# Kernel optimization log

Measured on AMD Instinct MI355X. Metric: run time of the kernel, lower is better.

Reference implementation:

```python
import jax, jax.numpy as jnp
import numpy as np

# OGB feature vocab sizes
ATOM_DIMS = [119, 4, 12, 12, 10, 6, 6, 2, 2]
BOND_DIMS = [5, 6, 2]
ATOM_OFF = np.concatenate([[0], np.cumsum(ATOM_DIMS)[:-1]]).astype(np.int32)
BOND_OFF = np.concatenate([[0], np.cumsum(BOND_DIMS)[:-1]]).astype(np.int32)
SCHEDULE_LEN = 5   # len(train_schedule) == len(eval_schedule)
NUM_GRAPHS = 12000
BN_EPS = 1e-5

N_NODES, N_EDGES, HIDDEN, NUM_TASKS = 300000, 600000, 128, 128


def setup_inputs() -> dict:
    key = jax.random.key(0)
    ks = jax.random.split(key, 16)
    x = jax.random.randint(ks[0], (N_NODES, 9), 0, 2, dtype=jnp.int32)
    edge_index = jax.random.randint(ks[1], (2, N_EDGES), 0, N_NODES, dtype=jnp.int32)
    edge_attr = jax.random.randint(ks[2], (N_EDGES, 3), 0, 2, dtype=jnp.int32)
    batch = jnp.sort(jax.random.randint(ks[3], (N_NODES,), 0, NUM_GRAPHS, dtype=jnp.int32))
    # learned parameters (embedding tables concatenated with offsets)
    atom_emb = jax.random.normal(ks[4], (sum(ATOM_DIMS), HIDDEN), jnp.float32) * 0.1
    bond_emb = jax.random.normal(ks[5], (sum(BOND_DIMS), HIDDEN), jnp.float32) * 0.1
    conv_W = jax.random.normal(ks[6], (HIDDEN, HIDDEN), jnp.float32) * (1.0 / np.sqrt(HIDDEN))
    conv_b = jnp.zeros((HIDDEN,), jnp.float32)
    root_emb = jax.random.normal(ks[7], (HIDDEN,), jnp.float32) * 0.1
    bn_gamma = jnp.ones((HIDDEN,), jnp.float32)
    bn_beta = jnp.zeros((HIDDEN,), jnp.float32)
    bn_mean = jnp.zeros((HIDDEN,), jnp.float32)   # running stats (eval mode)
    bn_var = jnp.ones((HIDDEN,), jnp.float32)
    lin_W = jax.random.normal(ks[8], (NUM_TASKS, HIDDEN), jnp.float32) * (1.0 / np.sqrt(HIDDEN))
    lin_b = jnp.zeros((NUM_TASKS,), jnp.float32)
    return {"x": x, "edge_index": edge_index, "edge_attr": edge_attr, "batch": batch,
            "atom_emb": atom_emb, "bond_emb": bond_emb, "conv_W": conv_W, "conv_b": conv_b,
            "root_emb": root_emb, "bn_gamma": bn_gamma, "bn_beta": bn_beta,
            "bn_mean": bn_mean, "bn_var": bn_var, "lin_W": lin_W, "lin_b": lin_b}


def reference(x, edge_index, edge_attr, batch, atom_emb, bond_emb, conv_W, conv_b,
              root_emb, bn_gamma, bn_beta, bn_mean, bn_var, lin_W, lin_b):
    N = x.shape[0]
    # AtomEncoder / BondEncoder: sum of per-feature embedding lookups
    h = atom_emb[x + jnp.asarray(ATOM_OFF, x.dtype)].sum(axis=1)            # [N, H]
    e = bond_emb[edge_attr + jnp.asarray(BOND_OFF, edge_attr.dtype)].sum(axis=1)  # [E, H]
    row, col = edge_index[0], edge_index[1]
    deg = jax.ops.segment_sum(jnp.ones_like(row, h.dtype), row, num_segments=N) + 1.0  # [N]
    dis = deg ** -0.5                                                        # deg >= 1, no inf
    norm = dis[row] * dis[col]                                               # [E]
    inv_std = bn_gamma / jnp.sqrt(bn_var + BN_EPS)
    for i in range(SCHEDULE_LEN):
        old = h
        z = h @ conv_W.T + conv_b                                            # [N, H]
        # message: norm * relu(x_j + edge_emb), aggregated at target (col) via scatter-add
        msg = norm[:, None] * jax.nn.relu(z[row] + e)                        # [E, H]
        agg = jax.ops.segment_sum(msg, col, num_segments=N)                  # [N, H]
        z = agg + jax.nn.relu(z + root_emb) / deg[:, None]                   # self-loop term
        z = jax.nn.relu(z)
        z = (z - bn_mean) * inv_std + bn_beta                                # BN (eval, running stats)
        # dropout: identity in eval mode
        # NOTE: faithful to source bug: smooth_fac is the loop index i, not schedule[i]
        h = i * old + (1 - i) * z
    # global mean pool over graphs
    counts = jax.ops.segment_sum(jnp.ones((N,), h.dtype), batch, num_segments=NUM_GRAPHS)
    pooled = jax.ops.segment_sum(h, batch, num_segments=NUM_GRAPHS) / jnp.maximum(counts, 1.0)[:, None]
    return pooled @ lin_W.T + lin_b                                          # [num_graphs, num_tasks]
```

## Files before the change

kernel.cpp:

```cpp
#include <hip/hip_runtime.h>

#define HID 128

typedef __attribute__((ext_vector_type(8))) short short8;
typedef __attribute__((ext_vector_type(8))) unsigned short ushort8v;
typedef __attribute__((ext_vector_type(4))) float floatx4;
typedef __attribute__((ext_vector_type(4))) unsigned short ushort4v;

__device__ __forceinline__ unsigned short f2bf(float f) {
    unsigned u = __builtin_bit_cast(unsigned, f);
    u += 0x7FFF + ((u >> 16) & 1);
    return (unsigned short)(u >> 16);
}
__device__ __forceinline__ float bf2f(unsigned short s) {
    unsigned u = ((unsigned)s) << 16;
    return __builtin_bit_cast(float, u);
}

__global__ void diag_kernel(float* __restrict__ out, long n, float val)
{
    long i = (long)blockIdx.x * blockDim.x + threadIdx.x;
    if (i < n) out[i] = val;
}

__global__ __launch_bounds__(256) void prep_kernel(
    float* __restrict__ dis, int* __restrict__ indeg, int N,
    const float* __restrict__ conv_W, unsigned short* __restrict__ Wb,
    const float* __restrict__ lin_W, unsigned short* __restrict__ linWb,
    const float* __restrict__ bond_emb, float* __restrict__ comb,
    const float* __restrict__ gamma, const float* __restrict__ beta,
    const float* __restrict__ mean, const float* __restrict__ var,
    float* __restrict__ bnsc, float* __restrict__ bnsh,
    const int* __restrict__ batch, int* __restrict__ gptr, int G, int B)
{
    int blk = blockIdx.x;
    int tid = threadIdx.x;
    if (blk < B) {
        int i = blk * 256 + tid;
        if (i < N) { dis[i] = 0.f; indeg[i] = 0; }
    } else if (blk < B + 64) {
        int i = (blk - B) * 256 + tid;
        Wb[i] = f2bf(conv_W[i]);
    } else if (blk < B + 128) {
        int i = (blk - B - 64) * 256 + tid;
        linWb[i] = f2bf(lin_W[i]);
    } else if (blk < B + 158) {
        int i = (blk - B - 128) * 2 + (tid >> 7);
        int c = tid & 127;
        int a0 = i / 12, a1 = (i % 12) / 2, a2 = i % 2;
        comb[i * HID + c] = bond_emb[a0 * HID + c] + bond_emb[(5 + a1) * HID + c]
                          + bond_emb[(11 + a2) * HID + c];
    } else if (blk == B + 158) {
        if (tid < HID) {
            float sc = gamma[tid] * rsqrtf(var[tid] + 1e-5f);
            bnsc[tid] = sc;
            bnsh[tid] = beta[tid] - mean[tid] * sc;
        }
    } else {
        int n = (blk - B - 159) * 256 + tid;
        if (n < N) {
            int b = batch[n];
            int bp = (n == 0) ? -1 : batch[n - 1];
            for (int g = bp + 1; g <= b; ++g) gptr[g] = n;
            if (n == N - 1)
                for (int g = b + 1; g <= G; ++g) gptr[g] = N;
        }
    }
}

__global__ void hist_kernel(const int* __restrict__ ei, float* __restrict__ dis,
                            int* __restrict__ indeg, int E)
{
    for (int e = blockIdx.x * blockDim.x + threadIdx.x; e < E; e += gridDim.x * blockDim.x) {
        atomicAdd(&dis[ei[e]], 1.f);
        atomicAdd(&indeg[ei[E + e]], 1);
    }
}

__global__ __launch_bounds__(256) void postdeg_kernel(
    float* __restrict__ dis, const int* __restrict__ indeg,
    int* __restrict__ partial, int N)
{
    __shared__ int s[256];
    int i = blockIdx.x * 256 + threadIdx.x;
    if (i < N) dis[i] = rsqrtf(dis[i] + 1.f);
    s[threadIdx.x] = (i < N) ? indeg[i] : 0;
    __syncthreads();
    for (int d = 128; d > 0; d >>= 1) {
        if (threadIdx.x < d) s[threadIdx.x] += s[threadIdx.x + d];
        __syncthreads();
    }
    if (threadIdx.x == 0) partial[blockIdx.x] = s[0];
}

__global__ __launch_bounds__(256) void scan1_kernel(
    const int* __restrict__ partial, int* __restrict__ offs,
    int* __restrict__ ptr, int B, int N)
{
    __shared__ int s[256];
    __shared__ int carry_s;
    int tid = threadIdx.x;
    if (tid == 0) carry_s = 0;
    __syncthreads();
    for (int base = 0; base < B; base += 256) {
        int i = base + tid;
        int v = (i < B) ? partial[i] : 0;
        s[tid] = v;
        __syncthreads();
        for (int d = 1; d < 256; d <<= 1) {
            int t = (tid >= d) ? s[tid - d] : 0;
            __syncthreads();
            s[tid] += t;
            __syncthreads();
        }
        int carry = carry_s;
        if (i < B) offs[i] = carry + s[tid] - v;
        __syncthreads();
        if (tid == 0) carry_s = carry + s[255];
        __syncthreads();
    }
    if (tid == 0) ptr[N] = carry_s;
}

__global__ __launch_bounds__(256) void scan2_kernel(
    const int* __restrict__ indeg, const int* __restrict__ offs,
    int* __restrict__ ptr, int* __restrict__ cursor, int N)
{
    __shared__ int s[256];
    int tid = threadIdx.x;
    int i = blockIdx.x * 256 + tid;
    int v = (i < N) ? indeg[i] : 0;
    s[tid] = v;
    __syncthreads();
    for (int d = 1; d < 256; d <<= 1) {
        int t = (tid >= d) ? s[tid - d] : 0;
        __syncthreads();
        s[tid] += t;
        __syncthreads();
    }
    if (i < N) {
        int ex = offs[blockIdx.x] + s[tid] - v;
        ptr[i] = ex;
        cursor[i] = ex;
    }
}

__global__ void fillcsr_kernel(const int* __restrict__ ei, const int* __restrict__ attr,
                               const float* __restrict__ dis, int* __restrict__ cursor,
                               int2* __restrict__ edata, int E)
{
    for (int e = blockIdx.x * blockDim.x + threadIdx.x; e < E; e += gridDim.x * blockDim.x) {
        int r   = ei[e];
        int col = ei[E + e];
        int pos = atomicAdd(&cursor[col], 1);
        int ci  = attr[e * 3] * 12 + attr[e * 3 + 1] * 2 + attr[e * 3 + 2];
        float nrm = dis[r] * dis[col];
        int2 ed;
        ed.x = r;
        ed.y = ci | ((int)f2bf(nrm) << 16);
        edata[pos] = ed;
    }
}

template<bool FIRST>
__device__ __forceinline__ ushort8v agg_node(
    long n, int c, const int* __restrict__ ptr, const int2* __restrict__ edata,
    const float* __restrict__ comb, const float* __restrict__ dis,
    const float* __restrict__ root, const float* __restrict__ bnsc,
    const float* __restrict__ bnsh, const unsigned short* __restrict__ zb,
    const unsigned short* __restrict__ hb, float fi)
{
    ushort8v zv = *reinterpret_cast<const ushort8v*>(zb + n * HID + c);
    ushort8v hv;
    if constexpr (!FIRST) hv = *reinterpret_cast<const ushort8v*>(hb + n * HID + c);
    float di = dis[n];
    float rd = di * di;
    float acc[8];
#pragma unroll
    for (int j = 0; j < 8; ++j) acc[j] = fmaxf(bf2f(zv[j]) + root[c + j], 0.f) * rd;

    int jb = ptr[n], je = ptr[n + 1];
    int j2 = jb;
    for (; j2 + 1 < je; j2 += 2) {
        int2 e0 = edata[j2];
        int2 e1 = edata[j2 + 1];
        ushort8v z0 = *reinterpret_cast<const ushort8v*>(zb + (long)e0.x * HID + c);
        ushort8v z1 = *reinterpret_cast<const ushort8v*>(zb + (long)e1.x * HID + c);
        const float* c0 = comb + (e0.y & 0xFF) * HID + c;
        const float* c1 = comb + (e1.y & 0xFF) * HID + c;
        float n0 = bf2f((unsigned short)(((unsigned)e0.y) >> 16));
        float n1 = bf2f((unsigned short)(((unsigned)e1.y) >> 16));
#pragma unroll
        for (int j = 0; j < 8; ++j) {
            acc[j] += fmaxf(bf2f(z0[j]) + c0[j], 0.f) * n0;
            acc[j] += fmaxf(bf2f(z1[j]) + c1[j], 0.f) * n1;
        }
    }
    if (j2 < je) {
        int2 e0 = edata[j2];
        ushort8v z0 = *reinterpret_cast<const ushort8v*>(zb + (long)e0.x * HID + c);
        const float* c0 = comb + (e0.y & 0xFF) * HID + c;
        float n0 = bf2f((unsigned short)(((unsigned)e0.y) >> 16));
#pragma unroll
        for (int j = 0; j < 8; ++j) acc[j] += fmaxf(bf2f(z0[j]) + c0[j], 0.f) * n0;
    }

    ushort8v o;
#pragma unroll
    for (int j = 0; j < 8; ++j) {
        float t = fmaxf(acc[j], 0.f) * bnsc[c + j] + bnsh[c + j];
        float h;
        if constexpr (FIRST) h = t;
        else h = fi * bf2f(hv[j]) + (1.f - fi) * t;
        o[j] = f2bf(h);
    }
    return o;
}

template<bool FIRST>
__global__ __launch_bounds__(256) void agg_kernel(
    const int* __restrict__ ptr, const int2* __restrict__ edata,
    const float* __restrict__ comb, const float* __restrict__ dis,
    const float* __restrict__ root, const float* __restrict__ bnsc,
    const float* __restrict__ bnsh, const unsigned short* __restrict__ zb,
    unsigned short* __restrict__ hb, float fi, int N)
{
    long n = (long)blockIdx.x * 16 + (threadIdx.x >> 4);
    if (n >= N) return;
    int c = (threadIdx.x & 15) * 8;
    ushort8v o = agg_node<FIRST>(n, c, ptr, edata, comb, dis, root, bnsc, bnsh, zb, hb, fi);
    *reinterpret_cast<ushort8v*>(hb + n * HID + c) = o;
}

__global__ __launch_bounds__(256) void gemm_kernel(
    const unsigned short* __restrict__ hb, const unsigned short* __restrict__ Wb,
    const float* __restrict__ bias, unsigned short* __restrict__ zb, int N)
{
    __shared__ unsigned short st[4][32][144];
    int tid = threadIdx.x;
    int wave = tid >> 6;
    int lane = tid & 63;
    int l15 = lane & 15;
    int q = lane >> 4;
    long row0 = (long)blockIdx.x * 128 + wave * 32;

    short8 a[2][4];
#pragma unroll
    for (int mt = 0; mt < 2; ++mt) {
        long rl = row0 + mt * 16 + l15;
        if (rl > (long)N - 1) rl = (long)N - 1;
        const unsigned short* ap = hb + rl * HID + q * 8;
#pragma unroll
        for (int kb = 0; kb < 4; ++kb)
            a[mt][kb] = *reinterpret_cast<const short8*>(ap + kb * 32);
    }

    floatx4 acc[2][8];
#pragma unroll
    for (int mt = 0; mt < 2; ++mt)
#pragma unroll
        for (int nt = 0; nt < 8; ++nt) {
            floatx4 zz = {0.f, 0.f, 0.f, 0.f};
            acc[mt][nt] = zz;
        }

#pragma unroll
    for (int nt = 0; nt < 8; ++nt) {
        const unsigned short* bp = Wb + (nt * 16 + l15) * HID + q * 8;
#pragma unroll
        for (int kb = 0; kb < 4; ++kb) {
            short8 b = *reinterpret_cast<const short8*>(bp + kb * 32);
            acc[0][nt] = __builtin_amdgcn_mfma_f32_16x16x32_bf16(a[0][kb], b, acc[0][nt], 0, 0, 0);
            acc[1][nt] = __builtin_amdgcn_mfma_f32_16x16x32_bf16(a[1][kb], b, acc[1][nt], 0, 0, 0);
        }
    }

    float bi[8];
#pragma unroll
    for (int nt = 0; nt < 8; ++nt) bi[nt] = bias[nt * 16 + l15];

#pragma unroll
    for (int mt = 0; mt < 2; ++mt)
#pragma unroll
        for (int r = 0; r < 4; ++r) {
            int lr = mt * 16 + q * 4 + r;
#pragma unroll
            for (int nt = 0; nt < 8; ++nt)
                st[wave][lr][l15 + 16 * nt] = f2bf(acc[mt][nt][r] + bi[nt]);
        }

#pragma unroll
    for (int it = 0; it < 8; ++it) {
        int lr = it * 4 + q;
        long gr = row0 + lr;
        if (gr < N) {
            ushort8v v = *reinterpret_cast<const ushort8v*>(&st[wave][lr][l15 * 8]);
            *reinterpret_cast<ushort8v*>(zb + gr * HID + l15 * 8) = v;
        }
    }
}

__global__ __launch_bounds__(256) void egemm_kernel(
    const int* __restrict__ x, const float* __restrict__ atom_emb,
    const unsigned short* __restrict__ Wb, const float* __restrict__ bias,
    unsigned short* __restrict__ zb, int N)
{
    __shared__ unsigned short st[4][32][144];
    int tid = threadIdx.x;
    int wave = tid >> 6;
    int lane = tid & 63;
    int l15 = lane & 15;
    int q = lane >> 4;
    long row0 = (long)blockIdx.x * 128 + wave * 32;
    const int OFF[9] = {0, 119, 123, 135, 147, 157, 163, 169, 171};

    int cc = l15 * 8;
#pragma unroll 1
    for (int s = 0; s < 8; ++s) {
        int lr = s * 4 + q;
        long n = row0 + lr;
        ushort8v o;
        if (n < N) {
            float acc[8];
#pragma unroll
            for (int j = 0; j < 8; ++j) acc[j] = 0.f;
#pragma unroll
            for (int f = 0; f < 9; ++f) {
                int idx = x[n * 9 + f] + OFF[f];
                const float* ep = atom_emb + (long)idx * HID + cc;
                floatx4 v0 = *reinterpret_cast<const floatx4*>(ep);
                floatx4 v1 = *reinterpret_cast<const floatx4*>(ep + 4);
#pragma unroll
                for (int j = 0; j < 4; ++j) { acc[j] += v0[j]; acc[j + 4] += v1[j]; }
            }
#pragma unroll
            for (int j = 0; j < 8; ++j) o[j] = f2bf(acc[j]);
        } else {
            ushort8v z8 = {0, 0, 0, 0, 0, 0, 0, 0};
            o = z8;
        }
        *reinterpret_cast<ushort8v*>(&st[wave][lr][cc]) = o;
    }

    short8 a[2][4];
#pragma unroll
    for (int mt = 0; mt < 2; ++mt) {
        int rl = mt * 16 + l15;
#pragma unroll
        for (int kb = 0; kb < 4; ++kb)
            a[mt][kb] = *reinterpret_cast<const short8*>(&st[wave][rl][q * 8 + kb * 32]);
    }

    floatx4 acc[2][8];
#pragma unroll
    for (int mt = 0; mt < 2; ++mt)
#pragma unroll
        for (int nt = 0; nt < 8; ++nt) {
            floatx4 zz = {0.f, 0.f, 0.f, 0.f};
            acc[mt][nt] = zz;
        }

#pragma unroll
    for (int nt = 0; nt < 8; ++nt) {
        const unsigned short* bp = Wb + (nt * 16 + l15) * HID + q * 8;
#pragma unroll
        for (int kb = 0; kb < 4; ++kb) {
            short8 b = *reinterpret_cast<const short8*>(bp + kb * 32);
            acc[0][nt] = __builtin_amdgcn_mfma_f32_16x16x32_bf16(a[0][kb], b, acc[0][nt], 0, 0, 0);
            acc[1][nt] = __builtin_amdgcn_mfma_f32_16x16x32_bf16(a[1][kb], b, acc[1][nt], 0, 0, 0);
        }
    }

    float bi[8];
#pragma unroll
    for (int nt = 0; nt < 8; ++nt) bi[nt] = bias[nt * 16 + l15];

#pragma unroll
    for (int mt = 0; mt < 2; ++mt)
#pragma unroll
        for (int r = 0; r < 4; ++r) {
            int lr = mt * 16 + q * 4 + r;
#pragma unroll
            for (int nt = 0; nt < 8; ++nt)
                st[wave][lr][l15 + 16 * nt] = f2bf(acc[mt][nt][r] + bi[nt]);
        }

#pragma unroll
    for (int it = 0; it < 8; ++it) {
        int lr = it * 4 + q;
        long gr = row0 + lr;
        if (gr < N) {
            ushort8v v = *reinterpret_cast<const ushort8v*>(&st[wave][lr][l15 * 8]);
            *reinterpret_cast<ushort8v*>(zb + gr * HID + l15 * 8) = v;
        }
    }
}

__global__ __launch_bounds__(256) void linmm_kernel(
    const unsigned short* __restrict__ pb, const unsigned short* __restrict__ Wb,
    const float* __restrict__ bias, float* __restrict__ out, int G)
{
    int wave = threadIdx.x >> 6;
    int lane = threadIdx.x & 63;
    int l15 = lane & 15;
    int q = lane >> 4;
    long row0 = (long)blockIdx.x * 128 + wave * 32;

    short8 a[2][4];
#pragma unroll
    for (int mt = 0; mt < 2; ++mt) {
        long rl = row0 + mt * 16 + l15;
        if (rl > (long)G - 1) rl = (long)G - 1;
        const unsigned short* ap = pb + rl * HID + q * 8;
#pragma unroll
        for (int kb = 0; kb < 4; ++kb)
            a[mt][kb] = *reinterpret_cast<const short8*>(ap + kb * 32);
    }

    floatx4 acc[2][8];
#pragma unroll
    for (int mt = 0; mt < 2; ++mt)
#pragma unroll
        for (int nt = 0; nt < 8; ++nt) {
            floatx4 zz = {0.f, 0.f, 0.f, 0.f};
            acc[mt][nt] = zz;
        }

#pragma unroll
    for (int nt = 0; nt < 8; ++nt) {
        const unsigned short* bp = Wb + (nt * 16 + l15) * HID + q * 8;
#pragma unroll
        for (int kb = 0; kb < 4; ++kb) {
            short8 b = *reinterpret_cast<const short8*>(bp + kb * 32);
            acc[0][nt] = __builtin_amdgcn_mfma_f32_16x16x32_bf16(a[0][kb], b, acc[0][nt], 0, 0, 0);
            acc[1][nt] = __builtin_amdgcn_mfma_f32_16x16x32_bf16(a[1][kb], b, acc[1][nt], 0, 0, 0);
        }
    }

    float bi[8];
#pragma unroll
    for (int nt = 0; nt < 8; ++nt) bi[nt] = bias[nt * 16 + l15];

#pragma unroll
    for (int mt = 0; mt < 2; ++mt)
#pragma unroll
        for (int r = 0; r < 4; ++r) {
            long rr = row0 + mt * 16 + q * 4 + r;
            if (rr < G) {
                float* op = out + rr * HID + l15;
#pragma unroll
                for (int nt = 0; nt < 8; ++nt)
                    op[nt * 16] = acc[mt][nt][r] + bi[nt];
            }
        }
}

__global__ __launch_bounds__(256) void pool_kernel(
    const unsigned short* __restrict__ hb, const int* __restrict__ gptr,
    unsigned short* __restrict__ pb, int G)
{
    int g = blockIdx.x;
    if (g >= G) return;
    int tid = threadIdx.x;
    int sub = tid >> 5;
    int c = (tid & 31) * 4;
    int lo = gptr[g], hi = gptr[g + 1];
    floatx4 s = {0.f, 0.f, 0.f, 0.f};
    for (int n = lo + sub; n < hi; n += 8) {
        ushort4v hv = *reinterpret_cast<const ushort4v*>(hb + (long)n * HID + c);
#pragma unroll
        for (int j = 0; j < 4; ++j) s[j] += bf2f(hv[j]);
    }
    __shared__ float ps[8][HID];
    *reinterpret_cast<floatx4*>(&ps[sub][c]) = s;
    __syncthreads();
    if (tid < HID) {
        float sum = 0.f;
#pragma unroll
        for (int k = 0; k < 8; ++k) sum += ps[k][tid];
        float cnt = (hi > lo) ? (float)(hi - lo) : 1.f;
        pb[(long)g * HID + tid] = f2bf(sum / cnt);
    }
}

extern "C" void kernel_launch(void* const* d_in, const int* in_sizes, int n_in,
                              void* d_out, int out_size, void* d_ws, size_t ws_size,
                              hipStream_t stream)
{
    const int* x          = (const int*)d_in[0];
    const int* ei         = (const int*)d_in[1];
    const int* attr       = (const int*)d_in[2];
    const int* batch      = (const int*)d_in[3];
    const float* atom_emb = (const float*)d_in[4];
    const float* bond_emb = (const float*)d_in[5];
    const float* conv_W   = (const float*)d_in[6];
    const float* conv_b   = (const float*)d_in[7];
    const float* root     = (const float*)d_in[8];
    const float* gamma    = (const float*)d_in[9];
    const float* beta     = (const float*)d_in[10];
    const float* mean     = (const float*)d_in[11];
    const float* var      = (const float*)d_in[12];
    const float* lin_W    = (const float*)d_in[13];
    const float* lin_b    = (const float*)d_in[14];
    float* out = (float*)d_out;

    const int N = in_sizes[0] / 9;
    const int E = in_sizes[1] / 2;
    const int G = out_size / HID;
    const int B = (N + 255) / 256;

    auto al = [](size_t b) { return (b + 255) & ~(size_t)255; };
    const size_t need =
        al((size_t)N * HID * 2) +
        al((size_t)N * HID * 2) +
        al((size_t)(N + 1) * 4) +
        al((size_t)E * 8) +
        al((size_t)N * 4) +
        al((size_t)2048 * 4) * 2 +
        al((size_t)(G + 1) * 4) +
        al((size_t)(G + 128) * HID * 2) +
        al((size_t)60 * HID * 4) +
        al((size_t)HID * 4) * 2 +
        al((size_t)HID * HID * 2) * 2;

    if (ws_size < need || B > 2048) {
        float v = (B > 2048) ? 3000.f : (1000.f + (float)(ws_size >> 20));
        long n = (long)out_size;
        diag_kernel<<<(int)((n + 255) / 256), 256, 0, stream>>>(out, n, v);
        return;
    }

    char* wsp = (char*)d_ws;
    size_t used = 0;
    auto alloc = [&](size_t bytes) { char* p = wsp + used; used += al(bytes); return p; };
    unsigned short* hb = (unsigned short*)alloc((size_t)N * HID * 2);
    unsigned short* zb = (unsigned short*)alloc((size_t)N * HID * 2);
    int* ptr      = (int*)alloc((size_t)(N + 1) * 4);
    int2* edata   = (int2*)alloc((size_t)E * 8);
    int* indeg    = (int*)alloc((size_t)N * 4);
    int* cursor   = indeg;
    int* partial  = (int*)alloc((size_t)2048 * 4);
    int* offs     = (int*)alloc((size_t)2048 * 4);
    int* gptr     = (int*)alloc((size_t)(G + 1) * 4);
    unsigned short* pb = (unsigned short*)alloc((size_t)(G + 128) * HID * 2);
    float* dis    = (float*)pb;
    float* comb   = (float*)alloc((size_t)60 * HID * 4);
    float* bnsc   = (float*)alloc((size_t)HID * 4);
    float* bnsh   = (float*)alloc((size_t)HID * 4);
    unsigned short* Wb    = (unsigned short*)alloc((size_t)HID * HID * 2);
    unsigned short* linWb = (unsigned short*)alloc((size_t)HID * HID * 2);

    prep_kernel<<<2 * B + 159, 256, 0, stream>>>(dis, indeg, N, conv_W, Wb, lin_W, linWb,
                                                 bond_emb, comb, gamma, beta, mean, var,
                                                 bnsc, bnsh, batch, gptr, G, B);
    hist_kernel<<<1024, 256, 0, stream>>>(ei, dis, indeg, E);
    postdeg_kernel<<<B, 256, 0, stream>>>(dis, indeg, partial, N);
    scan1_kernel<<<1, 256, 0, stream>>>(partial, offs, ptr, B, N);
    scan2_kernel<<<B, 256, 0, stream>>>(indeg, offs, ptr, cursor, N);
    fillcsr_kernel<<<1024, 256, 0, stream>>>(ei, attr, dis, cursor, edata, E);

    const int gemm_blocks = (N + 127) / 128;
    const int agg_blocks  = (N + 15) / 16;
    egemm_kernel<<<gemm_blocks, 256, 0, stream>>>(x, atom_emb, Wb, conv_b, zb, N);
    agg_kernel<true ><<<agg_blocks, 256, 0, stream>>>(ptr, edata, comb, dis, root,
            bnsc, bnsh, zb, hb, 0.f, N);
    const float fis[3] = {2.f, 3.f, 4.f};
    for (int t = 0; t < 3; ++t) {
        gemm_kernel<<<gemm_blocks, 256, 0, stream>>>(hb, Wb, conv_b, zb, N);
        agg_kernel<false><<<agg_blocks, 256, 0, stream>>>(ptr, edata, comb, dis, root,
                bnsc, bnsh, zb, hb, fis[t], N);
    }

    pool_kernel<<<G, 256, 0, stream>>>(hb, gptr, pb, G);
    linmm_kernel<<<(G + 127) / 128, 256, 0, stream>>>(pb, linWb, lin_b, out, G);
}
```

Before: 728.7 us.

## Permute hidden channel layout so MFMA results store directly without LDS transpose

```diff
diff --git a/kernel.cpp b/kernel.cpp
--- a/kernel.cpp
+++ b/kernel.cpp
@@ -1,6 +1,7 @@
 #include <hip/hip_runtime.h>
 
 #define HID 128
+#define ATOT 173
 
 typedef __attribute__((ext_vector_type(8))) short short8;
 typedef __attribute__((ext_vector_type(8))) unsigned short ushort8v;
@@ -16,6 +17,7 @@
     unsigned u = ((unsigned)s) << 16;
     return __builtin_bit_cast(float, u);
 }
+__device__ __forceinline__ int chact(int c) { return (c & 7) * 16 + (c >> 3); }
 
 __global__ void diag_kernel(float* __restrict__ out, long n, float val)
 {
@@ -31,6 +33,8 @@
     const float* __restrict__ gamma, const float* __restrict__ beta,
     const float* __restrict__ mean, const float* __restrict__ var,
     float* __restrict__ bnsc, float* __restrict__ bnsh,
+    const float* __restrict__ root, float* __restrict__ rootp,
+    const float* __restrict__ atom_emb, float* __restrict__ embp,
     const int* __restrict__ batch, int* __restrict__ gptr, int G, int B)
 {
     int blk = blockIdx.x;
@@ -40,24 +44,35 @@
         if (i < N) { dis[i] = 0.f; indeg[i] = 0; }
     } else if (blk < B + 64) {
         int i = (blk - B) * 256 + tid;
-        Wb[i] = f2bf(conv_W[i]);
+        int f = i >> 7, k = i & 127;
+        Wb[i] = f2bf(conv_W[f * HID + chact(k)]);
     } else if (blk < B + 128) {
         int i = (blk - B - 64) * 256 + tid;
-        linWb[i] = f2bf(lin_W[i]);
+        int t = i >> 7, k = i & 127;
+        linWb[i] = f2bf(lin_W[t * HID + chact(k)]);
     } else if (blk < B + 158) {
         int i = (blk - B - 128) * 2 + (tid >> 7);
         int c = tid & 127;
+        int ac = chact(c);
         int a0 = i / 12, a1 = (i % 12) / 2, a2 = i % 2;
-        comb[i * HID + c] = bond_emb[a0 * HID + c] + bond_emb[(5 + a1) * HID + c]
-                          + bond_emb[(11 + a2) * HID + c];
+        comb[i * HID + c] = bond_emb[a0 * HID + ac] + bond_emb[(5 + a1) * HID + ac]
+                          + bond_emb[(11 + a2) * HID + ac];
     } else if (blk == B + 158) {
         if (tid < HID) {
-            float sc = gamma[tid] * rsqrtf(var[tid] + 1e-5f);
+            int ac = chact(tid);
+            float sc = gamma[ac] * rsqrtf(var[ac] + 1e-5f);
             bnsc[tid] = sc;
-            bnsh[tid] = beta[tid] - mean[tid] * sc;
+            bnsh[tid] = beta[ac] - mean[ac] * sc;
+            rootp[tid] = root[ac];
+        }
+    } else if (blk < B + 246) {
+        int i = (blk - B - 159) * 256 + tid;
+        if (i < ATOT * HID) {
+            int r = i >> 7, c = i & 127;
+            embp[i] = atom_emb[r * HID + chact(c)];
         }
     } else {
-        int n = (blk - B - 159) * 256 + tid;
+        int n = (blk - B - 246) * 256 + tid;
         if (n < N) {
             int b = batch[n];
             int bp = (n == 0) ? -1 : batch[n - 1];
@@ -166,7 +181,7 @@
 __device__ __forceinline__ ushort8v agg_node(
     long n, int c, const int* __restrict__ ptr, const int2* __restrict__ edata,
     const float* __restrict__ comb, const float* __restrict__ dis,
-    const float* __restrict__ root, const float* __restrict__ bnsc,
+    const float* __restrict__ rootp, const float* __restrict__ bnsc,
     const float* __restrict__ bnsh, const unsigned short* __restrict__ zb,
     const unsigned short* __restrict__ hb, float fi)
 {
@@ -177,7 +192,7 @@
     float rd = di * di;
     float acc[8];
 #pragma unroll
-    for (int j = 0; j < 8; ++j) acc[j] = fmaxf(bf2f(zv[j]) + root[c + j], 0.f) * rd;
+    for (int j = 0; j < 8; ++j) acc[j] = fmaxf(bf2f(zv[j]) + rootp[c + j], 0.f) * rd;
 
     int jb = ptr[n], je = ptr[n + 1];
     int j2 = jb;
@@ -221,14 +236,14 @@
 __global__ __launch_bounds__(256) void agg_kernel(
     const int* __restrict__ ptr, const int2* __restrict__ edata,
     const float* __restrict__ comb, const float* __restrict__ dis,
-    const float* __restrict__ root, const float* __restrict__ bnsc,
+    const float* __restrict__ rootp, const float* __restrict__ bnsc,
     const float* __restrict__ bnsh, const unsigned short* __restrict__ zb,
     unsigned short* __restrict__ hb, float fi, int N)
 {
     long n = (long)blockIdx.x * 16 + (threadIdx.x >> 4);
     if (n >= N) return;
     int c = (threadIdx.x & 15) * 8;
-    ushort8v o = agg_node<FIRST>(n, c, ptr, edata, comb, dis, root, bnsc, bnsh, zb, hb, fi);
+    ushort8v o = agg_node<FIRST>(n, c, ptr, edata, comb, dis, rootp, bnsc, bnsh, zb, hb, fi);
     *reinterpret_cast<ushort8v*>(hb + n * HID + c) = o;
 }
 
@@ -236,7 +251,6 @@
     const unsigned short* __restrict__ hb, const unsigned short* __restrict__ Wb,
     const float* __restrict__ bias, unsigned short* __restrict__ zb, int N)
 {
-    __shared__ unsigned short st[4][32][144];
     int tid = threadIdx.x;
     int wave = tid >> 6;
     int lane = tid & 63;
@@ -283,29 +297,21 @@
     for (int mt = 0; mt < 2; ++mt)
 #pragma unroll
         for (int r = 0; r < 4; ++r) {
-            int lr = mt * 16 + q * 4 + r;
-#pragma unroll
-            for (int nt = 0; nt < 8; ++nt)
-                st[wave][lr][l15 + 16 * nt] = f2bf(acc[mt][nt][r] + bi[nt]);
-        }
-
-#pragma unroll
-    for (int it = 0; it < 8; ++it) {
-        int lr = it * 4 + q;
-        long gr = row0 + lr;
-        if (gr < N) {
-            ushort8v v = *reinterpret_cast<const ushort8v*>(&st[wave][lr][l15 * 8]);
-            *reinterpret_cast<ushort8v*>(zb + gr * HID + l15 * 8) = v;
-        }
-    }
+            long gr = row0 + mt * 16 + q * 4 + r;
+            if (gr < N) {
+                ushort8v o;
+#pragma unroll
+                for (int nt = 0; nt < 8; ++nt) o[nt] = f2bf(acc[mt][nt][r] + bi[nt]);
+                *reinterpret_cast<ushort8v*>(zb + gr * HID + l15 * 8) = o;
+            }
+        }
 }
 
 __global__ __launch_bounds__(256) void egemm_kernel(
-    const int* __restrict__ x, const float* __restrict__ atom_emb,
+    const int* __restrict__ x, const float* __restrict__ embp,
     const unsigned short* __restrict__ Wb, const float* __restrict__ bias,
     unsigned short* __restrict__ zb, int N)
 {
-    __shared__ unsigned short st[4][32][144];
     int tid = threadIdx.x;
     int wave = tid >> 6;
     int lane = tid & 63;
@@ -314,41 +320,38 @@
     long row0 = (long)blockIdx.x * 128 + wave * 32;
     const int OFF[9] = {0, 119, 123, 135, 147, 157, 163, 169, 171};
 
-    int cc = l15 * 8;
-#pragma unroll 1
-    for (int s = 0; s < 8; ++s) {
-        int lr = s * 4 + q;
-        long n = row0 + lr;
-        ushort8v o;
-        if (n < N) {
-            float acc[8];
-#pragma unroll
-            for (int j = 0; j < 8; ++j) acc[j] = 0.f;
-#pragma unroll
-            for (int f = 0; f < 9; ++f) {
-                int idx = x[n * 9 + f] + OFF[f];
-                const float* ep = atom_emb + (long)idx * HID + cc;
-                floatx4 v0 = *reinterpret_cast<const floatx4*>(ep);
-                floatx4 v1 = *reinterpret_cast<const floatx4*>(ep + 4);
-#pragma unroll
-                for (int j = 0; j < 4; ++j) { acc[j] += v0[j]; acc[j + 4] += v1[j]; }
+    short8 a[2][4];
+#pragma unroll
+    for (int mt = 0; mt < 2; ++mt) {
+        long rl = row0 + mt * 16 + l15;
+        if (rl > (long)N - 1) rl = (long)N - 1;
+        int xr[9];
+#pragma unroll
+        for (int f = 0; f < 9; ++f) xr[f] = x[rl * 9 + f] + OFF[f];
+        float s[32];
+#pragma unroll
+        for (int j = 0; j < 32; ++j) s[j] = 0.f;
+#pragma unroll
+        for (int f = 0; f < 9; ++f) {
+            const float* ep = embp + (long)xr[f] * HID + q * 8;
+#pragma unroll
+            for (int kb = 0; kb < 4; ++kb) {
+                floatx4 v0 = *reinterpret_cast<const floatx4*>(ep + kb * 32);
+                floatx4 v1 = *reinterpret_cast<const floatx4*>(ep + kb * 32 + 4);
+#pragma unroll
+                for (int j = 0; j < 4; ++j) {
+                    s[kb * 8 + j]     += v0[j];
+                    s[kb * 8 + 4 + j] += v1[j];
+                }
             }
-#pragma unroll
-            for (int j = 0; j < 8; ++j) o[j] = f2bf(acc[j]);
-        } else {
-            ushort8v z8 = {0, 0, 0, 0, 0, 0, 0, 0};
-            o = z8;
-        }
-        *reinterpret_cast<ushort8v*>(&st[wave][lr][cc]) = o;
-    }
-
-    short8 a[2][4];
-#pragma unroll
-    for (int mt = 0; mt < 2; ++mt) {
-        int rl = mt * 16 + l15;
-#pragma unroll
-        for (int kb = 0; kb < 4; ++kb)
-            a[mt][kb] = *reinterpret_cast<const short8*>(&st[wave][rl][q * 8 + kb * 32]);
+        }
+#pragma unroll
+        for (int kb = 0; kb < 4; ++kb) {
+            short8 v;
+#pragma unroll
+            for (int j = 0; j < 8; ++j) v[j] = (short)f2bf(s[kb * 8 + j]);
+            a[mt][kb] = v;
+        }
     }
 
     floatx4 acc[2][8];
@@ -379,21 +382,14 @@
     for (int mt = 0; mt < 2; ++mt)
 #pragma unroll
         for (int r = 0; r < 4; ++r) {
-            int lr = mt * 16 + q * 4 + r;
-#pragma unroll
-            for (int nt = 0; nt < 8; ++nt)
-                st[wave][lr][l15 + 16 * nt] = f2bf(acc[mt][nt][r] + bi[nt]);
-        }
-
-#pragma unroll
-    for (int it = 0; it < 8; ++it) {
-        int lr = it * 4 + q;
-        long gr = row0 + lr;
-        if (gr < N) {
-            ushort8v v = *reinterpret_cast<const ushort8v*>(&st[wave][lr][l15 * 8]);
-            *reinterpret_cast<ushort8v*>(zb + gr * HID + l15 * 8) = v;
-        }
-    }
+            long gr = row0 + mt * 16 + q * 4 + r;
+            if (gr < N) {
+                ushort8v o;
+#pragma unroll
+                for (int nt = 0; nt < 8; ++nt) o[nt] = f2bf(acc[mt][nt][r] + bi[nt]);
+                *reinterpret_cast<ushort8v*>(zb + gr * HID + l15 * 8) = o;
+            }
+        }
 }
 
 __global__ __launch_bounds__(256) void linmm_kernel(
@@ -520,7 +516,8 @@
         al((size_t)(G + 1) * 4) +
         al((size_t)(G + 128) * HID * 2) +
         al((size_t)60 * HID * 4) +
-        al((size_t)HID * 4) * 2 +
+        al((size_t)HID * 4) * 3 +
+        al((size_t)ATOT * HID * 4) +
         al((size_t)HID * HID * 2) * 2;
 
     if (ws_size < need || B > 2048) {
@@ -547,12 +544,15 @@
     float* comb   = (float*)alloc((size_t)60 * HID * 4);
     float* bnsc   = (float*)alloc((size_t)HID * 4);
     float* bnsh   = (float*)alloc((size_t)HID * 4);
+    float* rootp  = (float*)alloc((size_t)HID * 4);
+    float* embp   = (float*)alloc((size_t)ATOT * HID * 4);
     unsigned short* Wb    = (unsigned short*)alloc((size_t)HID * HID * 2);
     unsigned short* linWb = (unsigned short*)alloc((size_t)HID * HID * 2);
 
-    prep_kernel<<<2 * B + 159, 256, 0, stream>>>(dis, indeg, N, conv_W, Wb, lin_W, linWb,
+    prep_kernel<<<2 * B + 246, 256, 0, stream>>>(dis, indeg, N, conv_W, Wb, lin_W, linWb,
                                                  bond_emb, comb, gamma, beta, mean, var,
-                                                 bnsc, bnsh, batch, gptr, G, B);
+                                                 bnsc, bnsh, root, rootp, atom_emb, embp,
+                                                 batch, gptr, G, B);
     hist_kernel<<<1024, 256, 0, stream>>>(ei, dis, indeg, E);
     postdeg_kernel<<<B, 256, 0, stream>>>(dis, indeg, partial, N);
     scan1_kernel<<<1, 256, 0, stream>>>(partial, offs, ptr, B, N);
@@ -561,13 +561,13 @@
 
     const int gemm_blocks = (N + 127) / 128;
     const int agg_blocks  = (N + 15) / 16;
-    egemm_kernel<<<gemm_blocks, 256, 0, stream>>>(x, atom_emb, Wb, conv_b, zb, N);
-    agg_kernel<true ><<<agg_blocks, 256, 0, stream>>>(ptr, edata, comb, dis, root,
+    egemm_kernel<<<gemm_blocks, 256, 0, stream>>>(x, embp, Wb, conv_b, zb, N);
+    agg_kernel<true ><<<agg_blocks, 256, 0, stream>>>(ptr, edata, comb, dis, rootp,
             bnsc, bnsh, zb, hb, 0.f, N);
     const float fis[3] = {2.f, 3.f, 4.f};
     for (int t = 0; t < 3; ++t) {
         gemm_kernel<<<gemm_blocks, 256, 0, stream>>>(hb, Wb, conv_b, zb, N);
-        agg_kernel<false><<<agg_blocks, 256, 0, stream>>>(ptr, edata, comb, dis, root,
+        agg_kernel<false><<<agg_blocks, 256, 0, stream>>>(ptr, edata, comb, dis, rootp,
                 bnsc, bnsh, zb, hb, fis[t], N);
     }
 
```

After: 764.5 us. 4.9% more time.
